# Performance work log

Measured on AMD Instinct MI355X. Metric: run time of the kernel, lower is better.

## Reference

```python
import jax, jax.numpy as jnp
import numpy as np

B, V, C, D = 32, 64, 32, 256
VOCAB = 20000
NUM_T = 1000


def _run_lstm(x, Wih, Whh, b):
    # x: [T, B, H_in]; torch-style single-layer LSTM with zero initial state
    T, Bb, _ = x.shape
    H = Whh.shape[1]
    def step(carry, xt):
        h, c = carry
        z = xt @ Wih.T + h @ Whh.T + b
        i, f, g, o = jnp.split(z, 4, axis=-1)
        c = jax.nn.sigmoid(f) * c + jax.nn.sigmoid(i) * jnp.tanh(g)
        h = jax.nn.sigmoid(o) * jnp.tanh(c)
        return (h, c), h
    h0 = jnp.zeros((Bb, H), x.dtype)
    _, ys = jax.lax.scan(step, (h0, h0), x)
    return ys


def _forward(input_seqs, masks, lengths, seq_time_step, code_masks, emb, WQ1, WK1,
             decay, initial, lstm_Wih, lstm_Whh, lstm_b, hs_Wih, hs_Whh, hs_b,
             whk_W, whk_b, w1_W, w1_b, w2_W, w2_b, fuse_W, fuse_b, lab_W, lab_b,
             betas, Wdiff, diffusion_time_t, normal_noise):
    Bb, Vv, Cc = input_seqs.shape
    tok = input_seqs.reshape(-1, Cc)                      # [B*V, C]
    x = emb[tok]                                          # [B*V, C, D]
    q = x @ WQ1.T
    k = x @ WK1.T
    dp = jnp.einsum('bcd,bed->bce', q, k)                 # [B*V, C, C]
    cm = code_masks.reshape(-1, Cc)
    dp = dp - cm[:, None, :] - cm[:, :, None]
    sp = jax.nn.softmax(dp / jnp.sqrt(jnp.float32(D)), axis=-1)
    femb = jnp.einsum('bce,bed->bcd', sp, x)              # attended code embeddings
    femb = ((cm - 1e20) / -1e20)[:, :, None] * femb       # zero out padded codes
    dec = decay[tok][..., None]                           # [B*V, C, 1]
    ini = initial[tok][..., None]
    t = seq_time_step.reshape(-1)[:, None, None]          # [B*V, 1, 1]
    gate = jax.nn.sigmoid(dec * t + ini)                  # time-decay gate
    vv = jnp.einsum('bcx,bcd->bd', gate, femb)            # [B*V, D] visit vector
    vv = vv.reshape(Bb, Vv, -1).transpose(1, 0, 2)        # [V, B, D]

    lstm_out = _run_lstm(vv, lstm_Wih, lstm_Whh, lstm_b)  # [V, B, D]
    t_lstm = lstm_out.transpose(1, 0, 2)                  # [B, V, D]
    hiddenstate = _run_lstm(lstm_out, hs_Wih, hs_Whh, hs_b).transpose(1, 0, 2)

    # Vectorized form of the original per-step python loop.
    # NOTE: the original always uses e_k = t_lstm_out[:, 0:1, :] (step 0) -- kept faithfully.
    e_k = t_lstm[:, 0:1, :]                               # [B, 1, D]
    whp = hiddenstate[:, :-1, :] @ whk_W.T + whk_b        # [B, V-1, D]
    cat = jnp.concatenate([jnp.broadcast_to(e_k, whp.shape), whp], axis=-1)
    attn = jax.nn.softmax(jnp.tanh(cat @ w1_W.T + w1_b) @ w2_W.T + w2_b, axis=-1)
    rest = e_k * attn[..., 0:1] + whp * attn[..., 1:2]
    aligned = jnp.concatenate([e_k, rest], axis=1)        # [B, V, D]

    alpha = jnp.cumprod(1.0 - betas)[diffusion_time_t][:, None, None]
    noisy = aligned * jnp.sqrt(alpha) + normal_noise * jnp.sqrt(1.0 - alpha)
    predicted_noise = noisy @ Wdiff                       # surrogate for UNetModel (source not provided)
    gen = aligned + (normal_noise - predicted_noise)

    fused = jnp.concatenate([t_lstm, gen], axis=-1) @ fuse_W.T + fuse_b   # [B, V, D]
    mask_final = (jnp.arange(Vv)[None, :] == (lengths - 1)[:, None]).astype(fused.dtype)
    final = (fused * mask_final[:, :, None]).sum(axis=1)  # select last valid visit
    return final @ lab_W.T + lab_b                        # [B, 2]


def setup_inputs() -> dict:
    key = jax.random.key(0)
    ks = jax.random.split(key, 20)
    s = 0.05
    n = lambda i, shp: jax.random.normal(ks[i], shp, jnp.float32) * s
    emb = jax.random.normal(ks[0], (VOCAB + 1, D), jnp.float32) * 0.02
    emb = emb.at[VOCAB].set(0.0)  # padding_idx row
    return {
        'input_seqs': jax.random.randint(ks[1], (B, V, C), 0, VOCAB),
        'masks': jnp.zeros((B, V), jnp.float32),
        'lengths': jax.random.randint(ks[2], (B,), 1, V + 1),
        'seq_time_step': jax.random.uniform(ks[3], (B, V), jnp.float32),
        'code_masks': jnp.zeros((B, V, C), jnp.float32),
        'emb': emb,
        'WQ1': n(4, (D, D)), 'WK1': n(5, (D, D)),
        'decay': jnp.full((VOCAB + 1,), -0.1, jnp.float32),
        'initial': jnp.full((VOCAB + 1,), 1.0, jnp.float32),
        'lstm_Wih': n(6, (4 * D, D)), 'lstm_Whh': n(7, (4 * D, D)),
        'lstm_b': jnp.zeros((4 * D,), jnp.float32),
        'hs_Wih': n(8, (4 * D, D)), 'hs_Whh': n(9, (4 * D, D)),
        'hs_b': jnp.zeros((4 * D,), jnp.float32),
        'whk_W': n(10, (D, D)), 'whk_b': jnp.zeros((D,), jnp.float32),
        'w1_W': n(11, (64, 2 * D)), 'w1_b': jnp.zeros((64,), jnp.float32),
        'w2_W': n(12, (2, 64)), 'w2_b': jnp.zeros((2,), jnp.float32),
        'fuse_W': n(13, (D, 2 * D)), 'fuse_b': jnp.zeros((D,), jnp.float32),
        'lab_W': n(14, (2, D)), 'lab_b': jnp.zeros((2,), jnp.float32),
        'betas': jnp.linspace(1e-4, 0.02, NUM_T, dtype=jnp.float32),
        'Wdiff': n(15, (D, D)),
        'diffusion_time_t': jax.random.randint(ks[16], (B,), 0, NUM_T),
        'normal_noise': jax.random.normal(ks[17], (B, V, D), jnp.float32),
    }


def reference(input_seqs, masks, lengths, seq_time_step, code_masks, emb, WQ1, WK1,
              decay, initial, lstm_Wih, lstm_Whh, lstm_b, hs_Wih, hs_Whh, hs_b,
              whk_W, whk_b, w1_W, w1_b, w2_W, w2_b, fuse_W, fuse_b, lab_W, lab_b,
              betas, Wdiff, diffusion_time_t, normal_noise):
    return _forward(input_seqs, masks, lengths, seq_time_step, code_masks, emb, WQ1, WK1,
                    decay, initial, lstm_Wih, lstm_Whh, lstm_b, hs_Wih, hs_Whh, hs_b,
                    whk_W, whk_b, w1_W, w1_b, w2_W, w2_b, fuse_W, fuse_b, lab_W, lab_b,
                    betas, Wdiff, diffusion_time_t, normal_noise)
```

## Files before the change

### kernel.cpp

```cpp
#include <hip/hip_runtime.h>
#include <hip/hip_bf16.h>
#include <cmath>

typedef __attribute__((ext_vector_type(8))) short bf16x8;
typedef __attribute__((ext_vector_type(4))) float f32x4;
typedef __attribute__((ext_vector_type(4))) int i32x4;
typedef __attribute__((ext_vector_type(2))) unsigned int u32x2;

__device__ __forceinline__ float bf2f(unsigned short u) {
    unsigned int x = ((unsigned int)u) << 16;
    return __builtin_bit_cast(float, x);
}
__device__ __forceinline__ unsigned short f2bf(float f) {
    unsigned int x = __builtin_bit_cast(unsigned int, f);
    unsigned int lsb = (x >> 16) & 1u;
    x += 0x7fffu + lsb;
    return (unsigned short)(x >> 16);
}
__device__ __forceinline__ float sigm(float z) {
    return 1.f / (1.f + __expf(-z));
}
__device__ __forceinline__ float rcpf(float x) { return __builtin_amdgcn_rcpf(x); }
__device__ __forceinline__ float sigm_f(float z) { return rcpf(1.f + __expf(-z)); }
__device__ __forceinline__ float tanh_f(float z) { return 1.f - 2.f * rcpf(1.f + __expf(2.f * z)); }

__device__ __forceinline__ long ldg_sc8l(const void* p) {
    long r;
    asm volatile("global_load_dwordx2 %0, %1, off sc1" : "=v"(r) : "v"(p) : "memory");
    return r;
}
__device__ __forceinline__ u32x2 ldg_sc_u2(const void* p) {
    u32x2 r;
    asm volatile("global_load_dwordx2 %0, %1, off sc1" : "=v"(r) : "v"(p) : "memory");
    return r;
}
__device__ __forceinline__ void stg_sc_u2(void* p, u32x2 v) {
    asm volatile("global_store_dwordx2 %0, %1, off sc1" :: "v"(p), "v"(v) : "memory");
}
__device__ __forceinline__ void stg_sc_b(void* p, int v) {
    asm volatile("global_store_byte %0, %1, off sc1" :: "v"(p), "v"(v) : "memory");
}

__global__ void __launch_bounds__(256) pack_all(
    const float* __restrict__ Whh1, const float* __restrict__ Wih2,
    const float* __restrict__ Whh2, const float* __restrict__ Wih1,
    const float* __restrict__ WQ1, const float* __restrict__ WK1,
    const float* __restrict__ betas, const int* __restrict__ dift,
    const float* __restrict__ whk_W, const float* __restrict__ fuse_W,
    const float* __restrict__ w1_W,
    long* __restrict__ Wq, float* __restrict__ cs,
    unsigned short* __restrict__ W1h, unsigned short* __restrict__ M_pk,
    float* __restrict__ alpha, int* __restrict__ flags,
    float* __restrict__ whkT, float* __restrict__ fuseT,
    float* __restrict__ w1T) {
    int blk = blockIdx.x, tid = threadIdx.x;
    if (blk < 384) {
        int R = blk * 8 + (tid >> 5);
        int mat = R >> 10;
        int n = R & 1023;
        int t32 = tid & 31;
        const float* src = (mat == 0) ? Whh1 : (mat == 1 ? Wih2 : Whh2);
        const float* rp = src + (size_t)n * 256 + t32 * 8;
        float v[8];
        float mx = 0.f;
        for (int j = 0; j < 8; ++j) { v[j] = rp[j]; mx = fmaxf(mx, fabsf(v[j])); }
        for (int m = 1; m <= 16; m <<= 1) mx = fmaxf(mx, __shfl_xor(mx, m));
        float inv = mx > 0.f ? 127.f / mx : 0.f;
        unsigned int lo = 0, hi = 0;
        for (int j = 0; j < 4; ++j) {
            int iv = __float2int_rn(v[j] * inv);
            lo |= ((unsigned int)(unsigned char)(signed char)iv) << (8 * j);
            int iv2 = __float2int_rn(v[4 + j] * inv);
            hi |= ((unsigned int)(unsigned char)(signed char)iv2) << (8 * j);
        }
        int g = n >> 8, rem = n & 255;
        int w8 = rem >> 5, dt = (rem >> 4) & 1, cc = rem & 15;
        int t8 = g * 2 + dt;
        int kb = t32 >> 2, q = t32 & 3;
        unsigned int* dst = (unsigned int*)Wq +
            ((size_t)((mat * 512 + w8 * 64 + t8 * 8 + kb) * 64) + q * 16 + cc) * 2;
        dst[0] = lo;
        dst[1] = hi;
        if (t32 == 0) cs[mat * 1024 + n] = mx / 16129.f;
    } else if (blk < 512) {
        int cch = (blk - 384) * 256 + tid;
        int nt = cch >> 9;
        int r = cch & 511;
        int kb = r >> 6;
        int lane = r & 63;
        int grow = nt * 16 + (lane & 15);
        int k0 = kb * 32 + (lane >> 4) * 8;
        const float* sp = Wih1 + (size_t)grow * 256 + k0;
        bf16x8 hi;
        for (int j = 0; j < 8; ++j) hi[j] = (short)f2bf(sp[j]);
        *reinterpret_cast<bf16x8*>(W1h + (size_t)cch * 8) = hi;
    } else if (blk == 512) {
        if (tid < 32) {
            int tb = dift[tid];
            float p = 1.f;
            for (int i = 0; i <= tb; ++i) p *= (1.f - betas[i]);
            alpha[tid] = p;
        }
    } else if (blk == 513) {
        for (int i = tid; i < 4096; i += 256) flags[i] = 0;
    } else if (blk < 578) {
        int gid = (blk - 514) * 256 + tid;
        for (int i = 0; i < 4; ++i) {
            int e = gid + i * 16384;
            int k = e >> 8, dd = e & 255;
            whkT[e] = whk_W[(size_t)dd * 256 + k];
        }
    } else if (blk < 706) {
        int gid = (blk - 578) * 256 + tid;
        for (int i = 0; i < 4; ++i) {
            int e = gid + i * 32768;
            int k = e >> 8, dd = e & 255;
            fuseT[e] = fuse_W[(size_t)dd * 512 + k];
        }
    } else if (blk < 738) {
        int gid = (blk - 706) * 256 + tid;
        for (int i = 0; i < 4; ++i) {
            int e = gid + i * 8192;
            int k = e >> 6, j = e & 63;
            w1T[e] = w1_W[(size_t)j * 512 + k];
        }
    } else {
        __shared__ unsigned short As[256][32];
        __shared__ unsigned short Bs[256][32];
        int bx = blk - 738;
        int e0 = (bx >> 3) << 5;
        int f0 = (bx & 7) << 5;
        int col = tid & 31, rr = tid >> 5;
        for (int rep = 0; rep < 32; ++rep) {
            int d = rep * 8 + rr;
            As[d][col] = f2bf(WQ1[d * 256 + e0 + col]);
            Bs[d][col] = f2bf(WK1[d * 256 + f0 + col]);
        }
        __syncthreads();
        int el = tid & 31;
        int fl0 = tid >> 5;
        for (int i = 0; i < 4; ++i) {
            int fl = fl0 + 8 * i;
            float acc = 0.f;
            for (int d = 0; d < 256; ++d)
                acc += bf2f(As[d][el]) * bf2f(Bs[d][fl]);
            int e = e0 + el, f = f0 + fl;
            int kb = e >> 5, r = (e >> 3) & 3, j = e & 7;
            int nb = f >> 4;
            int lane = (r << 4) | (f & 15);
            M_pk[(((nb * 8 + kb) * 64) + lane) * 8 + j] = f2bf(acc);
        }
    }
}

__global__ void __launch_bounds__(256) eprep(const float* __restrict__ emb,
                                             const unsigned short* __restrict__ M_pk,
                                             unsigned short* __restrict__ Ep) {
    __shared__ __align__(16) unsigned short x_bf[32 * 256];
    int v0 = blockIdx.x * 32;
    int tid = threadIdx.x;
    for (int it = 0; it < 8; ++it) {
        int fidx = it * 256 + tid;
        int cc = fidx >> 6;
        int f4 = fidx & 63;
        int row = v0 + cc;
        float4 vx = make_float4(0.f, 0.f, 0.f, 0.f);
        if (row < 20001)
            vx = *(reinterpret_cast<const float4*>(emb + (size_t)row * 256) + f4);
        int colx = f4 * 4;
        ushort4 w;
        w.x = f2bf(vx.x); w.y = f2bf(vx.y); w.z = f2bf(vx.z); w.w = f2bf(vx.w);
        *reinterpret_cast<ushort4*>(&x_bf[cc * 256 + (colx ^ ((cc & 7) << 3))]) = w;
    }
    __syncthreads();
    int wv = tid >> 6, lane = tid & 63, lr = lane & 15, lk = lane >> 4;
    f32x4 acc[2][4];
    for (int a = 0; a < 2; ++a)
        for (int n = 0; n < 4; ++n) acc[a][n] = (f32x4){0.f, 0.f, 0.f, 0.f};
    for (int kb = 0; kb < 8; ++kb) {
        bf16x8 afr[2];
        for (int mb = 0; mb < 2; ++mb) {
            int row = mb * 16 + lr;
            int colx = kb * 32 + lk * 8;
            afr[mb] = *reinterpret_cast<const bf16x8*>(&x_bf[row * 256 + (colx ^ ((row & 7) << 3))]);
        }
        for (int nbi = 0; nbi < 4; ++nbi) {
            int nb = wv * 4 + nbi;
            bf16x8 bfr = *reinterpret_cast<const bf16x8*>(M_pk + (((nb * 8 + kb) * 64) + lane) * 8);
            acc[0][nbi] = __builtin_amdgcn_mfma_f32_16x16x32_bf16(afr[0], bfr, acc[0][nbi], 0, 0, 0);
            acc[1][nbi] = __builtin_amdgcn_mfma_f32_16x16x32_bf16(afr[1], bfr, acc[1][nbi], 0, 0, 0);
        }
    }
    for (int mb = 0; mb < 2; ++mb)
        for (int nbi = 0; nbi < 4; ++nbi)
            for (int r = 0; r < 4; ++r) {
                int row = mb * 16 + lk * 4 + r;
                int col = wv * 64 + nbi * 16 + lr;
                if (v0 + row < 20001)
                    Ep[(size_t)(v0 + row) * 256 + col] = f2bf(acc[mb][nbi][r]);
            }
}

__global__ void __launch_bounds__(256) attn_bags(
    const int* __restrict__ seqs, const float* __restrict__ tstep,
    const float* __restrict__ cmask, const float* __restrict__ emb,
    const float* __restrict__ decay, const float* __restrict__ initial,
    const unsigned short* __restrict__ Ep, float* __restrict__ vv) {
    __shared__ __align__(16) unsigned short x_bf[32 * 256];
    __shared__ __align__(16) unsigned short t1_bf[32 * 256];
    __shared__ float dp_f[32 * 33];
    __shared__ float gate_sh[32];
    __shared__ float cm_sh[32];
    __shared__ int tok_sh[32];
    __shared__ float w_sh[32];

    int bag = blockIdx.x;
    int tid = threadIdx.x;

    if (tid < 32) {
        int tok = seqs[bag * 32 + tid];
        tok_sh[tid] = tok;
        float cm = cmask[bag * 32 + tid];
        cm_sh[tid] = cm;
        float tt = tstep[bag];
        float g = sigm(decay[tok] * tt + initial[tok]);
        g *= (cm - 1e20f) / (-1e20f);
        gate_sh[tid] = g;
    }
    __syncthreads();

    for (int it = 0; it < 8; ++it) {
        int fidx = it * 256 + tid;
        int c = fidx >> 6;
        int f4 = fidx & 63;
        const float4* src = reinterpret_cast<const float4*>(emb + (size_t)tok_sh[c] * 256) + f4;
        float4 vx = *src;
        int colx = f4 * 4;
        int eidx = c * 256 + (colx ^ ((c & 7) << 3));
        ushort4 w;
        w.x = f2bf(vx.x); w.y = f2bf(vx.y); w.z = f2bf(vx.z); w.w = f2bf(vx.w);
        *reinterpret_cast<ushort4*>(&x_bf[eidx]) = w;
    }
    for (int it = 0; it < 4; ++it) {
        int idx = it * 256 + tid;
        int cc = idx >> 5;
        int colx = (idx & 31) * 8;
        bf16x8 e = *reinterpret_cast<const bf16x8*>(Ep + (size_t)tok_sh[cc] * 256 + colx);
        *reinterpret_cast<bf16x8*>(&t1_bf[cc * 256 + (colx ^ ((cc & 7) << 3))]) = e;
    }
    __syncthreads();

    int wv = tid >> 6;
    int lane = tid & 63;
    int lr = lane & 15;
    int lk = lane >> 4;

    {
        int mb = wv >> 1, nb2 = wv & 1;
        f32x4 dacc = (f32x4){0.f, 0.f, 0.f, 0.f};
        for (int kb = 0; kb < 8; ++kb) {
            int cola = kb * 32 + lk * 8;
            int rowa = mb * 16 + lr;
            bf16x8 afr = *reinterpret_cast<const bf16x8*>(&t1_bf[rowa * 256 + (cola ^ ((rowa & 7) << 3))]);
            int rowb = nb2 * 16 + lr;
            bf16x8 bfr = *reinterpret_cast<const bf16x8*>(&x_bf[rowb * 256 + (cola ^ ((rowb & 7) << 3))]);
            dacc = __builtin_amdgcn_mfma_f32_16x16x32_bf16(afr, bfr, dacc, 0, 0, 0);
        }
        for (int r = 0; r < 4; ++r) {
            int c = mb * 16 + lk * 4 + r;
            int e = nb2 * 16 + lr;
            dp_f[c * 33 + e] = dacc[r];
        }
    }
    __syncthreads();

    if (tid < 32) {
        int c = tid;
        float cmc = cm_sh[c];
        float lg[32];
        float mx = -1e30f;
        for (int e = 0; e < 32; ++e) {
            float l = (dp_f[c * 33 + e] - cmc - cm_sh[e]) * 0.0625f;
            lg[e] = l;
            mx = fmaxf(mx, l);
        }
        float s = 0.f;
        for (int e = 0; e < 32; ++e) { float ex = __expf(lg[e] - mx); lg[e] = ex; s += ex; }
        float inv = 1.f / s;
        for (int e = 0; e < 32; ++e) dp_f[c * 33 + e] = lg[e] * inv;
    }
    __syncthreads();
    if (tid < 32) {
        int e = tid;
        float a2 = 0.f;
        for (int c = 0; c < 32; ++c) a2 += gate_sh[c] * dp_f[c * 33 + e];
        w_sh[e] = a2;
    }
    __syncthreads();

    float accv = 0.f;
    int d = tid;
    for (int e = 0; e < 32; ++e)
        accv += w_sh[e] * bf2f(x_bf[e * 256 + (d ^ ((e & 7) << 3))]);
    vv[(size_t)bag * 256 + d] = accv;
}

__global__ void __launch_bounds__(256) x1_mfma(const float* __restrict__ vv,
                                               const unsigned short* __restrict__ W1h,
                                               const float* __restrict__ lstm_b,
                                               unsigned short* __restrict__ X1bf) {
    __shared__ __align__(16) unsigned short xs[32 * 256];
    int blk = blockIdx.x;
    int rb = blk >> 3, gb = blk & 7;
    int tid = threadIdx.x;
    for (int it = 0; it < 8; ++it) {
        int idx = it * 256 + tid;
        int row = idx >> 6, f4 = idx & 63;
        float4 v = *reinterpret_cast<const float4*>(vv + (size_t)(rb * 32 + row) * 256 + f4 * 4);
        ushort4 w;
        w.x = f2bf(v.x); w.y = f2bf(v.y); w.z = f2bf(v.z); w.w = f2bf(v.w);
        *reinterpret_cast<ushort4*>(&xs[row * 256 + ((f4 * 4) ^ ((row & 7) << 3))]) = w;
    }
    __syncthreads();
    int wv = tid >> 6, lane = tid & 63, cl = lane & 15, kh = lane >> 4;
    f32x4 acc[2][2];
    for (int n = 0; n < 2; ++n) {
        int nt = gb * 8 + wv * 2 + n;
        float bz = lstm_b[nt * 16 + cl];
        acc[n][0] = (f32x4){bz, bz, bz, bz};
        acc[n][1] = (f32x4){bz, bz, bz, bz};
    }
    #pragma unroll
    for (int kb = 0; kb < 8; ++kb) {
        int k = kb * 32 + kh * 8;
        bf16x8 a0 = *reinterpret_cast<const bf16x8*>(&xs[cl * 256 + (k ^ ((cl & 7) << 3))]);
        bf16x8 a1 = *reinterpret_cast<const bf16x8*>(&xs[(16 + cl) * 256 + (k ^ (((16 + cl) & 7) << 3))]);
        for (int n = 0; n < 2; ++n) {
            int nt = gb * 8 + wv * 2 + n;
            size_t o = ((size_t)(nt * 8 + kb) * 64 + lane) * 8;
            bf16x8 bh = *reinterpret_cast<const bf16x8*>(W1h + o);
            acc[n][0] = __builtin_amdgcn_mfma_f32_16x16x32_bf16(a0, bh, acc[n][0], 0, 0, 0);
            acc[n][1] = __builtin_amdgcn_mfma_f32_16x16x32_bf16(a1, bh, acc[n][1], 0, 0, 0);
        }
    }
    for (int n = 0; n < 2; ++n) {
        int nt = gb * 8 + wv * 2 + n;
        int g = nt * 16 + cl;
        int dX = g & 255, gt = g >> 8;
        for (int mt = 0; mt < 2; ++mt)
            for (int r = 0; r < 4; ++r) {
                int row = rb * 32 + mt * 16 + kh * 4 + r;
                int b = row >> 6, t = row & 63;
                X1bf[((size_t)t * 32 + b) * 1024 + dX * 4 + gt] = f2bf(acc[n][mt][r]);
            }
    }
}

__global__ void __launch_bounds__(512, 2) lstm_persist(
    const long* __restrict__ Wq, const float* __restrict__ cs,
    const unsigned short* __restrict__ X1bf, const float* __restrict__ hs_b,
    unsigned short* __restrict__ h1bf, unsigned short* __restrict__ h2bf,
    signed char* h1q, unsigned short* p1, int* flags) {
    int role = blockIdx.x;
    int half = role & 1;
    int kind = role >> 1;
    int tid = threadIdx.x;
    int w = tid >> 6, lane = tid & 63, c = lane & 15, q = lane >> 4;

    long wt[64];
    #pragma unroll
    for (int t8 = 0; t8 < 8; ++t8)
        #pragma unroll
        for (int kb = 0; kb < 8; ++kb)
            wt[t8 * 8 + kb] = Wq[(size_t)((kind * 512 + w * 64 + t8 * 8 + kb) * 64) + lane];
    float csv[8];
    #pragma unroll
    for (int t8 = 0; t8 < 8; ++t8) {
        int g = t8 >> 1, dt = t8 & 1;
        csv[t8] = cs[kind * 1024 + g * 256 + w * 32 + dt * 16 + c];
    }

    if (kind == 0) {
        __shared__ signed char hq[2][16][272];
        float cstate[8] = {0.f, 0.f, 0.f, 0.f, 0.f, 0.f, 0.f, 0.f};
        int B0 = half * 16 + q * 4;
        int dbase = w * 32;
        for (int t = 0; t < 64; ++t) {
            ushort4 xv[8];
            #pragma unroll
            for (int dt = 0; dt < 2; ++dt)
                #pragma unroll
                for (int r = 0; r < 4; ++r) {
                    int B = B0 + r, d = dbase + dt * 16 + c;
                    xv[dt * 4 + r] = *reinterpret_cast<const ushort4*>(
                        X1bf + ((size_t)(t * 32 + B) * 1024 + d * 4));
                }
            i32x4 acc[8];
            #pragma unroll
            for (int i = 0; i < 8; ++i) acc[i] = (i32x4){0, 0, 0, 0};
            if (t > 0) {
                int pb = (t - 1) & 1;
                long a[8];
                #pragma unroll
                for (int kb = 0; kb < 8; ++kb)
                    a[kb] = *reinterpret_cast<const long*>(&hq[pb][c][kb * 32 + q * 8]);
                #pragma unroll
                for (int t8 = 0; t8 < 8; ++t8)
                    #pragma unroll
                    for (int kb = 0; kb < 8; ++kb)
                        acc[t8] = __builtin_amdgcn_mfma_i32_16x16x32_i8(
                            a[kb], wt[t8 * 8 + kb], acc[t8], 0, 0, 0);
            }
            #pragma unroll
            for (int dt = 0; dt < 2; ++dt)
                #pragma unroll
                for (int r = 0; r < 4; ++r) {
                    int idx = dt * 4 + r;
                    ushort4 x = xv[idx];
                    float zi = (float)acc[0 + dt][r] * csv[0 + dt] + bf2f(x.x);
                    float zf = (float)acc[2 + dt][r] * csv[2 + dt] + bf2f(x.y);
                    float zg = (float)acc[4 + dt][r] * csv[4 + dt] + bf2f(x.z);
                    float zo = (float)acc[6 + dt][r] * csv[6 + dt] + bf2f(x.w);
                    float cn = sigm_f(zf) * cstate[idx] + sigm_f(zi) * tanh_f(zg);
                    float hn = sigm_f(zo) * tanh_f(cn);
                    cstate[idx] = cn;
                    int B = B0 + r, d = dbase + dt * 16 + c;
                    h1bf[(size_t)(t * 32 + B) * 256 + d] = f2bf(hn);
                    int hv = __float2int_rn(hn * 127.f);
                    hq[t & 1][q * 4 + r][d] = (signed char)hv;
                    stg_sc_b(h1q + (size_t)(t * 32 + B) * 256 + d, hv);
                }
            asm volatile("s_waitcnt vmcnt(0)" ::: "memory");
            if (lane == 0)
                __hip_atomic_store(flags + t * 16 + half * 8 + w, 1,
                                   __ATOMIC_RELAXED, __HIP_MEMORY_SCOPE_AGENT);
            __syncthreads();
        }
    } else if (kind == 1) {
        for (int s = 0; s < 64; ++s) {
            const int* f = flags + s * 16 + half * 8;
            while (1) {
                int v = 1;
                if (lane < 8)
                    v = __hip_atomic_load(f + lane, __ATOMIC_RELAXED, __HIP_MEMORY_SCOPE_AGENT);
                if (__all(v != 0)) break;
                __builtin_amdgcn_s_sleep(1);
            }
            __builtin_amdgcn_sched_barrier(0);
            const signed char* hb = h1q + (size_t)(s * 32 + half * 16) * 256;
            long a[8];
            #pragma unroll
            for (int kb = 0; kb < 8; ++kb)
                a[kb] = ldg_sc8l(hb + c * 256 + kb * 32 + q * 8);
            asm volatile("s_waitcnt vmcnt(0)" ::: "memory");
            __builtin_amdgcn_sched_barrier(0);
            i32x4 acc[8];
            #pragma unroll
            for (int i = 0; i < 8; ++i) acc[i] = (i32x4){0, 0, 0, 0};
            #pragma unroll
            for (int t8 = 0; t8 < 8; ++t8)
                #pragma unroll
                for (int kb = 0; kb < 8; ++kb)
                    acc[t8] = __builtin_amdgcn_mfma_i32_16x16x32_i8(
                        a[kb], wt[t8 * 8 + kb], acc[t8], 0, 0, 0);
            #pragma unroll
            for (int t8 = 0; t8 < 8; ++t8) {
                int g = t8 >> 1, dt = t8 & 1;
                int n = g * 256 + w * 32 + dt * 16 + c;
                u32x2 pv;
                pv.x = (unsigned int)f2bf((float)acc[t8][0] * csv[t8]) |
                       ((unsigned int)f2bf((float)acc[t8][1] * csv[t8]) << 16);
                pv.y = (unsigned int)f2bf((float)acc[t8][2] * csv[t8]) |
                       ((unsigned int)f2bf((float)acc[t8][3] * csv[t8]) << 16);
                stg_sc_u2(p1 + ((size_t)(s * 2 + half) * 1024 + n) * 16 + q * 4, pv);
            }
            asm volatile("s_waitcnt vmcnt(0)" ::: "memory");
            if (lane == 0)
                __hip_atomic_store(flags + 1024 + s * 16 + half * 8 + w, 1,
                                   __ATOMIC_RELAXED, __HIP_MEMORY_SCOPE_AGENT);
        }
    } else {
        __shared__ signed char hq2[2][16][272];
        float cstate[8] = {0.f, 0.f, 0.f, 0.f, 0.f, 0.f, 0.f, 0.f};
        float bias[8];
        #pragma unroll
        for (int t8 = 0; t8 < 8; ++t8) {
            int g = t8 >> 1, dt = t8 & 1;
            bias[t8] = hs_b[g * 256 + w * 32 + dt * 16 + c];
        }
        int B0 = half * 16 + q * 4;
        int dbase = w * 32;
        for (int s = 0; s < 64; ++s) {
            const int* fp = flags + 1024 + s * 16 + half * 8 + w;
            while (__hip_atomic_load(fp, __ATOMIC_RELAXED, __HIP_MEMORY_SCOPE_AGENT) == 0)
                __builtin_amdgcn_s_sleep(1);
            __builtin_amdgcn_sched_barrier(0);
            u32x2 pv[8];
            #pragma unroll
            for (int t8 = 0; t8 < 8; ++t8) {
                int g = t8 >> 1, dt = t8 & 1;
                int n = g * 256 + w * 32 + dt * 16 + c;
                pv[t8] = ldg_sc_u2(p1 + ((size_t)(s * 2 + half) * 1024 + n) * 16 + q * 4);
            }
            i32x4 acc[8];
            #pragma unroll
            for (int i = 0; i < 8; ++i) acc[i] = (i32x4){0, 0, 0, 0};
            if (s > 0) {
                int pb = (s - 1) & 1;
                long a[8];
                #pragma unroll
                for (int kb = 0; kb < 8; ++kb)
                    a[kb] = *reinterpret_cast<const long*>(&hq2[pb][c][kb * 32 + q * 8]);
                asm volatile("s_waitcnt vmcnt(0)" ::: "memory");
                __builtin_amdgcn_sched_barrier(0);
                #pragma unroll
                for (int t8 = 0; t8 < 8; ++t8)
                    #pragma unroll
                    for (int kb = 0; kb < 8; ++kb)
                        acc[t8] = __builtin_amdgcn_mfma_i32_16x16x32_i8(
                            a[kb], wt[t8 * 8 + kb], acc[t8], 0, 0, 0);
            } else {
                asm volatile("s_waitcnt vmcnt(0)" ::: "memory");
                __builtin_amdgcn_sched_barrier(0);
            }
            #pragma unroll
            for (int dt = 0; dt < 2; ++dt)
                #pragma unroll
                for (int r = 0; r < 4; ++r) {
                    int idx = dt * 4 + r;
                    float p_i = bf2f((unsigned short)((r < 2 ? pv[0 + dt].x : pv[0 + dt].y) >> ((r & 1) * 16)));
                    float p_f = bf2f((unsigned short)((r < 2 ? pv[2 + dt].x : pv[2 + dt].y) >> ((r & 1) * 16)));
                    float p_g = bf2f((unsigned short)((r < 2 ? pv[4 + dt].x : pv[4 + dt].y) >> ((r & 1) * 16)));
                    float p_o = bf2f((unsigned short)((r < 2 ? pv[6 + dt].x : pv[6 + dt].y) >> ((r & 1) * 16)));
                    float zi = (float)acc[0 + dt][r] * csv[0 + dt] + p_i + bias[0 + dt];
                    float zf = (float)acc[2 + dt][r] * csv[2 + dt] + p_f + bias[2 + dt];
                    float zg = (float)acc[4 + dt][r] * csv[4 + dt] + p_g + bias[4 + dt];
                    float zo = (float)acc[6 + dt][r] * csv[6 + dt] + p_o + bias[6 + dt];
                    float cn = sigm_f(zf) * cstate[idx] + sigm_f(zi) * tanh_f(zg);
                    float hn = sigm_f(zo) * tanh_f(cn);
                    cstate[idx] = cn;
                    int B = B0 + r, d = dbase + dt * 16 + c;
                    h2bf[(size_t)(s * 32 + B) * 256 + d] = f2bf(hn);
                    hq2[s & 1][q * 4 + r][d] = (signed char)__float2int_rn(hn * 127.f);
                }
            __syncthreads();
        }
    }
}

__global__ void __launch_bounds__(256) tail_k(
    const int* __restrict__ lengths,
    const unsigned short* __restrict__ h1, const unsigned short* __restrict__ h2,
    const float* __restrict__ whkT, const float* __restrict__ whk_b,
    const float* __restrict__ w1T, const float* __restrict__ w1_b,
    const float* __restrict__ w2_W, const float* __restrict__ w2_b,
    const float* __restrict__ fuseT, const float* __restrict__ fuse_b,
    const float* __restrict__ lab_W, const float* __restrict__ lab_b,
    const float* __restrict__ Wdiff, const float* __restrict__ alpha,
    const float* __restrict__ noise, float* __restrict__ out) {
    __shared__ float ek[256], tv[256], hs[256], whp[256], a1s[64];
    __shared__ float noisy_s[256], fin[512], fused_s[256], attn_s[2];
    int b = blockIdx.x, tid = threadIdx.x;
    int vstar = lengths[b] - 1;
    {
        ek[tid] = bf2f(h1[(size_t)b * 256 + tid]);
        tv[tid] = bf2f(h1[((size_t)vstar * 32 + b) * 256 + tid]);
        if (vstar > 0)
            hs[tid] = bf2f(h2[((size_t)(vstar - 1) * 32 + b) * 256 + tid]);
    }
    __syncthreads();

    float aligned;
    if (vstar > 0) {
        float s0 = 0.f, s1 = 0.f, s2 = 0.f, s3 = 0.f;
        for (int k = 0; k < 256; k += 4) {
            s0 += whkT[(k + 0) * 256 + tid] * hs[k + 0];
            s1 += whkT[(k + 1) * 256 + tid] * hs[k + 1];
            s2 += whkT[(k + 2) * 256 + tid] * hs[k + 2];
            s3 += whkT[(k + 3) * 256 + tid] * hs[k + 3];
        }
        whp[tid] = whk_b[tid] + s0 + s1 + s2 + s3;
        __syncthreads();
        if (tid < 64) {
            float a0 = 0.f, a1 = 0.f, a2 = 0.f, a3 = 0.f;
            for (int k = 0; k < 256; k += 4) {
                a0 += w1T[(k + 0) * 64 + tid] * ek[k + 0];
                a1 += w1T[(k + 1) * 64 + tid] * ek[k + 1];
                a2 += w1T[(k + 2) * 64 + tid] * ek[k + 2];
                a3 += w1T[(k + 3) * 64 + tid] * ek[k + 3];
            }
            for (int k = 0; k < 256; k += 4) {
                a0 += w1T[(256 + k + 0) * 64 + tid] * whp[k + 0];
                a1 += w1T[(256 + k + 1) * 64 + tid] * whp[k + 1];
                a2 += w1T[(256 + k + 2) * 64 + tid] * whp[k + 2];
                a3 += w1T[(256 + k + 3) * 64 + tid] * whp[k + 3];
            }
            a1s[tid] = tanhf(w1_b[tid] + a0 + a1 + a2 + a3);
        }
        __syncthreads();
        if (tid < 2) {
            float a3 = w2_b[tid];
            const float* wr2 = w2_W + tid * 64;
            for (int k = 0; k < 64; ++k) a3 += wr2[k] * a1s[k];
            attn_s[tid] = a3;
        }
        __syncthreads();
        float m = fmaxf(attn_s[0], attn_s[1]);
        float e0 = __expf(attn_s[0] - m), e1 = __expf(attn_s[1] - m);
        float inv = 1.f / (e0 + e1);
        aligned = ek[tid] * (e0 * inv) + whp[tid] * (e1 * inv);
    } else {
        aligned = ek[tid];
    }

    float al = alpha[b];
    float sa = sqrtf(al), sb = sqrtf(1.f - al);
    float nz = noise[((size_t)b * 64 + vstar) * 256 + tid];
    noisy_s[tid] = aligned * sa + nz * sb;
    __syncthreads();
    {
        float p0 = 0.f, p1v = 0.f, p2 = 0.f, p3 = 0.f;
        for (int k = 0; k < 256; k += 4) {
            p0 += noisy_s[k + 0] * Wdiff[(size_t)(k + 0) * 256 + tid];
            p1v += noisy_s[k + 1] * Wdiff[(size_t)(k + 1) * 256 + tid];
            p2 += noisy_s[k + 2] * Wdiff[(size_t)(k + 2) * 256 + tid];
            p3 += noisy_s[k + 3] * Wdiff[(size_t)(k + 3) * 256 + tid];
        }
        float gen = aligned + nz - (p0 + p1v + p2 + p3);
        fin[tid] = tv[tid];
        fin[256 + tid] = gen;
    }
    __syncthreads();
    {
        float f0 = 0.f, f1 = 0.f, f2 = 0.f, f3 = 0.f;
        for (int k = 0; k < 512; k += 4) {
            f0 += fuseT[(k + 0) * 256 + tid] * fin[k + 0];
            f1 += fuseT[(k + 1) * 256 + tid] * fin[k + 1];
            f2 += fuseT[(k + 2) * 256 + tid] * fin[k + 2];
            f3 += fuseT[(k + 3) * 256 + tid] * fin[k + 3];
        }
        fused_s[tid] = fuse_b[tid] + f0 + f1 + f2 + f3;
    }
    __syncthreads();
    if (tid < 2) {
        float o = lab_b[tid];
        const float* lw = lab_W + tid * 256;
        for (int k = 0; k < 256; ++k) o += lw[k] * fused_s[k];
        out[b * 2 + tid] = o;
    }
}

extern "C" void kernel_launch(void* const* d_in, const int* in_sizes, int n_in,
                              void* d_out, int out_size, void* d_ws, size_t ws_size,
                              hipStream_t stream) {
    const int*   seqs    = (const int*)  d_in[0];
    const int*   lengths = (const int*)  d_in[2];
    const float* tstep   = (const float*)d_in[3];
    const float* cmask   = (const float*)d_in[4];
    const float* emb     = (const float*)d_in[5];
    const float* WQ1     = (const float*)d_in[6];
    const float* WK1     = (const float*)d_in[7];
    const float* decay   = (const float*)d_in[8];
    const float* initial = (const float*)d_in[9];
    const float* Wih1    = (const float*)d_in[10];
    const float* Whh1    = (const float*)d_in[11];
    const float* lstm_b  = (const float*)d_in[12];
    const float* Wih2    = (const float*)d_in[13];
    const float* Whh2    = (const float*)d_in[14];
    const float* hs_b    = (const float*)d_in[15];
    const float* whk_W   = (const float*)d_in[16];
    const float* whk_b   = (const float*)d_in[17];
    const float* w1_W    = (const float*)d_in[18];
    const float* w1_b    = (const float*)d_in[19];
    const float* w2_W    = (const float*)d_in[20];
    const float* w2_b    = (const float*)d_in[21];
    const float* fuse_W  = (const float*)d_in[22];
    const float* fuse_b  = (const float*)d_in[23];
    const float* lab_W   = (const float*)d_in[24];
    const float* lab_b   = (const float*)d_in[25];
    const float* betas   = (const float*)d_in[26];
    const float* Wdiff   = (const float*)d_in[27];
    const int*   dift    = (const int*)  d_in[28];
    const float* noise   = (const float*)d_in[29];
    float* out = (float*)d_out;

    float* ws = (float*)d_ws;
    size_t off = 0;
    auto alloc = [&](size_t nfloats) { size_t r = off; off += (nfloats + 63) & ~(size_t)63; return r; };
    unsigned short* M_pk  = (unsigned short*)(ws + alloc(32768));
    float*          alpha = ws + alloc(64);
    float*          cs    = ws + alloc(3072);
    int*            flags = (int*)(ws + alloc(4096));
    float*          vv    = ws + alloc(524288);
    unsigned short* X1bf  = (unsigned short*)(ws + alloc(1048576));
    unsigned short* h1bf  = (unsigned short*)(ws + alloc(262144));
    unsigned short* h2bf  = (unsigned short*)(ws + alloc(262144));
    unsigned short* p1    = (unsigned short*)(ws + alloc(1048576));
    long*           Wq    = (long*)(ws + alloc(196608));
    unsigned short* W1h   = (unsigned short*)(ws + alloc(131072));
    float*          whkT  = ws + alloc(65536);
    float*          fuseT = ws + alloc(131072);
    float*          w1T   = ws + alloc(32768);
    signed char*    h1q   = (signed char*)(ws + alloc(131072));
    unsigned short* Ep    = (unsigned short*)(ws + alloc(2560128));

    pack_all<<<802, 256, 0, stream>>>(Whh1, Wih2, Whh2, Wih1, WQ1, WK1, betas, dift,
                                      whk_W, fuse_W, w1_W,
                                      Wq, cs, W1h, M_pk, alpha, flags,
                                      whkT, fuseT, w1T);
    eprep<<<626, 256, 0, stream>>>(emb, M_pk, Ep);
    attn_bags<<<2048, 256, 0, stream>>>(seqs, tstep, cmask, emb, decay, initial, Ep, vv);
    x1_mfma<<<512, 256, 0, stream>>>(vv, W1h, lstm_b, X1bf);
    lstm_persist<<<6, 512, 0, stream>>>(Wq, cs, X1bf, hs_b, h1bf, h2bf, h1q, p1, flags);
    tail_k<<<32, 256, 0, stream>>>(lengths, h1bf, h2bf, whkT, whk_b,
                                   w1T, w1_b, w2_W, w2_b, fuseT, fuse_b,
                                   lab_W, lab_b, Wdiff, alpha, noise, out);
}
```

Before: 350.4 us.

## Prefetch next-step LSTM inputs in persistent pipeline and store only needed hidden states

```diff
diff --git a/kernel.cpp b/kernel.cpp
--- a/kernel.cpp
+++ b/kernel.cpp
@@ -356,9 +356,10 @@
     }
 }
 
-__global__ void __launch_bounds__(512, 2) lstm_persist(
+__global__ void __launch_bounds__(512, 1) lstm_persist(
     const long* __restrict__ Wq, const float* __restrict__ cs,
     const unsigned short* __restrict__ X1bf, const float* __restrict__ hs_b,
+    const int* __restrict__ lengths,
     unsigned short* __restrict__ h1bf, unsigned short* __restrict__ h2bf,
     signed char* h1q, unsigned short* p1, int* flags) {
     int role = blockIdx.x;
@@ -385,6 +386,9 @@
         float cstate[8] = {0.f, 0.f, 0.f, 0.f, 0.f, 0.f, 0.f, 0.f};
         int B0 = half * 16 + q * 4;
         int dbase = w * 32;
+        int vstar[4];
+        #pragma unroll
+        for (int r = 0; r < 4; ++r) vstar[r] = lengths[B0 + r] - 1;
         for (int t = 0; t < 64; ++t) {
             ushort4 xv[8];
             #pragma unroll
@@ -425,7 +429,8 @@
                     float hn = sigm_f(zo) * tanh_f(cn);
                     cstate[idx] = cn;
                     int B = B0 + r, d = dbase + dt * 16 + c;
-                    h1bf[(size_t)(t * 32 + B) * 256 + d] = f2bf(hn);
+                    if (t == 0 || t == vstar[r])
+                        h1bf[(size_t)(t * 32 + B) * 256 + d] = f2bf(hn);
                     int hv = __float2int_rn(hn * 127.f);
                     hq[t & 1][q * 4 + r][d] = (signed char)hv;
                     stg_sc_b(h1q + (size_t)(t * 32 + B) * 256 + d, hv);
@@ -437,8 +442,9 @@
             __syncthreads();
         }
     } else if (kind == 1) {
-        for (int s = 0; s < 64; ++s) {
-            const int* f = flags + s * 16 + half * 8;
+        long acur[8], anext[8];
+        {
+            const int* f = flags + half * 8;
             while (1) {
                 int v = 1;
                 if (lane < 8)
@@ -447,13 +453,29 @@
                 __builtin_amdgcn_s_sleep(1);
             }
             __builtin_amdgcn_sched_barrier(0);
-            const signed char* hb = h1q + (size_t)(s * 32 + half * 16) * 256;
-            long a[8];
+            const signed char* hb = h1q + (size_t)(half * 16) * 256;
             #pragma unroll
             for (int kb = 0; kb < 8; ++kb)
-                a[kb] = ldg_sc8l(hb + c * 256 + kb * 32 + q * 8);
+                acur[kb] = ldg_sc8l(hb + c * 256 + kb * 32 + q * 8);
             asm volatile("s_waitcnt vmcnt(0)" ::: "memory");
             __builtin_amdgcn_sched_barrier(0);
+        }
+        for (int s = 0; s < 64; ++s) {
+            if (s < 63) {
+                const int* f = flags + (s + 1) * 16 + half * 8;
+                while (1) {
+                    int v = 1;
+                    if (lane < 8)
+                        v = __hip_atomic_load(f + lane, __ATOMIC_RELAXED, __HIP_MEMORY_SCOPE_AGENT);
+                    if (__all(v != 0)) break;
+                    __builtin_amdgcn_s_sleep(1);
+                }
+                __builtin_amdgcn_sched_barrier(0);
+                const signed char* hb = h1q + (size_t)((s + 1) * 32 + half * 16) * 256;
+                #pragma unroll
+                for (int kb = 0; kb < 8; ++kb)
+                    anext[kb] = ldg_sc8l(hb + c * 256 + kb * 32 + q * 8);
+            }
             i32x4 acc[8];
             #pragma unroll
             for (int i = 0; i < 8; ++i) acc[i] = (i32x4){0, 0, 0, 0};
@@ -462,7 +484,7 @@
                 #pragma unroll
                 for (int kb = 0; kb < 8; ++kb)
                     acc[t8] = __builtin_amdgcn_mfma_i32_16x16x32_i8(
-                        a[kb], wt[t8 * 8 + kb], acc[t8], 0, 0, 0);
+                        acur[kb], wt[t8 * 8 + kb], acc[t8], 0, 0, 0);
             #pragma unroll
             for (int t8 = 0; t8 < 8; ++t8) {
                 int g = t8 >> 1, dt = t8 & 1;
@@ -475,9 +497,12 @@
                 stg_sc_u2(p1 + ((size_t)(s * 2 + half) * 1024 + n) * 16 + q * 4, pv);
             }
             asm volatile("s_waitcnt vmcnt(0)" ::: "memory");
+            __builtin_amdgcn_sched_barrier(0);
             if (lane == 0)
                 __hip_atomic_store(flags + 1024 + s * 16 + half * 8 + w, 1,
                                    __ATOMIC_RELAXED, __HIP_MEMORY_SCOPE_AGENT);
+            #pragma unroll
+            for (int kb = 0; kb < 8; ++kb) acur[kb] = anext[kb];
         }
     } else {
         __shared__ signed char hq2[2][16][272];
@@ -490,18 +515,39 @@
         }
         int B0 = half * 16 + q * 4;
         int dbase = w * 32;
-        for (int s = 0; s < 64; ++s) {
-            const int* fp = flags + 1024 + s * 16 + half * 8 + w;
+        int vstar[4];
+        #pragma unroll
+        for (int r = 0; r < 4; ++r) vstar[r] = lengths[B0 + r] - 1;
+        u32x2 pvc[8], pvn[8];
+        {
+            const int* fp = flags + 1024 + half * 8 + w;
             while (__hip_atomic_load(fp, __ATOMIC_RELAXED, __HIP_MEMORY_SCOPE_AGENT) == 0)
                 __builtin_amdgcn_s_sleep(1);
             __builtin_amdgcn_sched_barrier(0);
-            u32x2 pv[8];
             #pragma unroll
             for (int t8 = 0; t8 < 8; ++t8) {
                 int g = t8 >> 1, dt = t8 & 1;
                 int n = g * 256 + w * 32 + dt * 16 + c;
-                pv[t8] = ldg_sc_u2(p1 + ((size_t)(s * 2 + half) * 1024 + n) * 16 + q * 4);
-            }
+                pvc[t8] = ldg_sc_u2(p1 + ((size_t)half * 1024 + n) * 16 + q * 4);
+            }
+        }
+        for (int s = 0; s < 64; ++s) {
+            if (s < 63) {
+                const int* fp = flags + 1024 + (s + 1) * 16 + half * 8 + w;
+                while (__hip_atomic_load(fp, __ATOMIC_RELAXED, __HIP_MEMORY_SCOPE_AGENT) == 0)
+                    __builtin_amdgcn_s_sleep(1);
+                __builtin_amdgcn_sched_barrier(0);
+                #pragma unroll
+                for (int t8 = 0; t8 < 8; ++t8) {
+                    int g = t8 >> 1, dt = t8 & 1;
+                    int n = g * 256 + w * 32 + dt * 16 + c;
+                    pvn[t8] = ldg_sc_u2(p1 + ((size_t)((s + 1) * 2 + half) * 1024 + n) * 16 + q * 4);
+                }
+                asm volatile("s_waitcnt vmcnt(8)" ::: "memory");
+            } else {
+                asm volatile("s_waitcnt vmcnt(0)" ::: "memory");
+            }
+            __builtin_amdgcn_sched_barrier(0);
             i32x4 acc[8];
             #pragma unroll
             for (int i = 0; i < 8; ++i) acc[i] = (i32x4){0, 0, 0, 0};
@@ -511,27 +557,22 @@
                 #pragma unroll
                 for (int kb = 0; kb < 8; ++kb)
                     a[kb] = *reinterpret_cast<const long*>(&hq2[pb][c][kb * 32 + q * 8]);
-                asm volatile("s_waitcnt vmcnt(0)" ::: "memory");
-                __builtin_amdgcn_sched_barrier(0);
                 #pragma unroll
                 for (int t8 = 0; t8 < 8; ++t8)
                     #pragma unroll
                     for (int kb = 0; kb < 8; ++kb)
                         acc[t8] = __builtin_amdgcn_mfma_i32_16x16x32_i8(
                             a[kb], wt[t8 * 8 + kb], acc[t8], 0, 0, 0);
-            } else {
-                asm volatile("s_waitcnt vmcnt(0)" ::: "memory");
-                __builtin_amdgcn_sched_barrier(0);
             }
             #pragma unroll
             for (int dt = 0; dt < 2; ++dt)
                 #pragma unroll
                 for (int r = 0; r < 4; ++r) {
                     int idx = dt * 4 + r;
-                    float p_i = bf2f((unsigned short)((r < 2 ? pv[0 + dt].x : pv[0 + dt].y) >> ((r & 1) * 16)));
-                    float p_f = bf2f((unsigned short)((r < 2 ? pv[2 + dt].x : pv[2 + dt].y) >> ((r & 1) * 16)));
-                    float p_g = bf2f((unsigned short)((r < 2 ? pv[4 + dt].x : pv[4 + dt].y) >> ((r & 1) * 16)));
-                    float p_o = bf2f((unsigned short)((r < 2 ? pv[6 + dt].x : pv[6 + dt].y) >> ((r & 1) * 16)));
+                    float p_i = bf2f((unsigned short)((r < 2 ? pvc[0 + dt].x : pvc[0 + dt].y) >> ((r & 1) * 16)));
+                    float p_f = bf2f((unsigned short)((r < 2 ? pvc[2 + dt].x : pvc[2 + dt].y) >> ((r & 1) * 16)));
+                    float p_g = bf2f((unsigned short)((r < 2 ? pvc[4 + dt].x : pvc[4 + dt].y) >> ((r & 1) * 16)));
+                    float p_o = bf2f((unsigned short)((r < 2 ? pvc[6 + dt].x : pvc[6 + dt].y) >> ((r & 1) * 16)));
                     float zi = (float)acc[0 + dt][r] * csv[0 + dt] + p_i + bias[0 + dt];
                     float zf = (float)acc[2 + dt][r] * csv[2 + dt] + p_f + bias[2 + dt];
                     float zg = (float)acc[4 + dt][r] * csv[4 + dt] + p_g + bias[4 + dt];
@@ -540,10 +581,13 @@
                     float hn = sigm_f(zo) * tanh_f(cn);
                     cstate[idx] = cn;
                     int B = B0 + r, d = dbase + dt * 16 + c;
-                    h2bf[(size_t)(s * 32 + B) * 256 + d] = f2bf(hn);
+                    if (s == vstar[r] - 1)
+                        h2bf[(size_t)(s * 32 + B) * 256 + d] = f2bf(hn);
                     hq2[s & 1][q * 4 + r][d] = (signed char)__float2int_rn(hn * 127.f);
                 }
             __syncthreads();
+            #pragma unroll
+            for (int t8 = 0; t8 < 8; ++t8) pvc[t8] = pvn[t8];
         }
     }
 }
@@ -711,7 +755,8 @@
     eprep<<<626, 256, 0, stream>>>(emb, M_pk, Ep);
     attn_bags<<<2048, 256, 0, stream>>>(seqs, tstep, cmask, emb, decay, initial, Ep, vv);
     x1_mfma<<<512, 256, 0, stream>>>(vv, W1h, lstm_b, X1bf);
-    lstm_persist<<<6, 512, 0, stream>>>(Wq, cs, X1bf, hs_b, h1bf, h2bf, h1q, p1, flags);
+    lstm_persist<<<6, 512, 0, stream>>>(Wq, cs, X1bf, hs_b, lengths,
+                                        h1bf, h2bf, h1q, p1, flags);
     tail_k<<<32, 256, 0, stream>>>(lengths, h1bf, h2bf, whkT, whk_b,
                                    w1T, w1_b, w2_W, w2_b, fuseT, fuse_b,
                                    lab_W, lab_b, Wdiff, alpha, noise, out);
```

Result: slower. 365.3 us (+4.3%).
